# Kernel tuning notes

Measured on AMD Instinct MI355X. Metric: run time of the kernel, lower is better.

The kernel has to match this reference:

```python
import jax, jax.numpy as jnp
import numpy as np

# Segment boundaries from the original hard-coded slices: 13,13,13,9,4 repeated twice
SEG_BOUNDS = [0, 13, 26, 39, 48, 52, 65, 78, 91, 100, 104]


def segmented_log_softmax(x):
    # x: [B, 104]; independent log-softmax over each of the 10 fixed segments
    return jnp.concatenate(
        [jax.nn.log_softmax(x[:, a:b], axis=-1)
         for a, b in zip(SEG_BOUNDS[:-1], SEG_BOUNDS[1:])], axis=-1)


def setup_inputs() -> dict:
    key = jax.random.key(0)
    ks = jax.random.split(key, 8)
    B, H, D = 8192, 2048, 104
    return {
        "line": jax.random.normal(ks[0], (B, D), dtype=jnp.float32),
        "hidden": jax.random.normal(ks[1], (B, H), dtype=jnp.float32),
        "U_w": jax.random.normal(ks[2], (H, H), dtype=jnp.float32) * 0.02,
        "U_b": jax.random.normal(ks[3], (H,), dtype=jnp.float32) * 0.02,
        "W_w": jax.random.normal(ks[4], (H, D), dtype=jnp.float32) * 0.02,
        "W_b": jax.random.normal(ks[5], (H,), dtype=jnp.float32) * 0.02,
        "V_w": jax.random.normal(ks[6], (D, H), dtype=jnp.float32) * 0.02,
        "V_b": jax.random.normal(ks[7], (D,), dtype=jnp.float32) * 0.02,
    }


def reference(line, hidden, U_w, U_b, W_w, W_b, V_w, V_b):
    # h_t = sigmoid(U(hidden) + W(line)); torch Linear: y = x @ W.T + b
    h_t = jax.nn.sigmoid(hidden @ U_w.T + U_b + line @ W_w.T + W_b)  # [B, H]
    pred = h_t @ V_w.T + V_b                                          # [B, 104]
    pred_logsoft = segmented_log_softmax(pred)                        # [B, 104]
    return pred_logsoft, h_t
```

## Files before the change

kernel.cpp:

```cpp
#include <hip/hip_runtime.h>
#include <cstdint>
#include <cstddef>


typedef __bf16 bf16x8 __attribute__((ext_vector_type(8)));
typedef float  f32x4  __attribute__((ext_vector_type(4)));
typedef float  f32x16 __attribute__((ext_vector_type(16)));
typedef int    i32x8  __attribute__((ext_vector_type(8)));
typedef unsigned short ushort8 __attribute__((ext_vector_type(8)));
typedef unsigned char  uchar8  __attribute__((ext_vector_type(8)));
typedef float  float4v __attribute__((ext_vector_type(4)));

#define BB 8192
#define HH 2048
#define DD 104

static __device__ __forceinline__ unsigned short f2bf(float f) {
  unsigned u = __float_as_uint(f);
  unsigned r = (u + 0x7FFFu + ((u >> 16) & 1u)) >> 16;
  return (unsigned short)r;
}

static __device__ __forceinline__ unsigned char f2fp8(float x) {
  unsigned u = __float_as_uint(x);
  unsigned s = (u >> 24) & 0x80u;
  float ax = fabsf(x);
  ax = fminf(ax, 448.0f);
  unsigned code;
  if (ax >= 0.015625f) {
    unsigned b = __float_as_uint(ax);
    unsigned lsb = (b >> 20) & 1u;
    b += 0x0007FFFFu + lsb;
    unsigned e = (b >> 23) & 0xFFu;
    code = ((e - 120u) << 3) | ((b >> 20) & 7u);
  } else {
    code = (unsigned)__float2int_rn(ax * 512.0f);
  }
  return (unsigned char)(s | code);
}

#define GLD_LDS(g, l)                                                          \
  __builtin_amdgcn_global_load_lds(                                            \
      (__attribute__((address_space(1))) void*)(g),                            \
      (__attribute__((address_space(3))) void*)(l), 16, 0, 0)

#define MEMFENCE asm volatile("" ::: "memory")
#define MFMA16(a, b, c) __builtin_amdgcn_mfma_f32_16x16x32_bf16((a), (b), (c), 0, 0, 0)

__global__ __launch_bounds__(256) void conv_fp8_kernel(
    const float* __restrict__ hidden, const float* __restrict__ Uw,
    unsigned char* __restrict__ out_h, unsigned char* __restrict__ out_u) {
  long long i = ((long long)blockIdx.x * blockDim.x + threadIdx.x) * 8;
  const float* src; unsigned char* dst; long long off;
  if (i < (long long)BB * HH) { src = hidden; dst = out_h; off = i; }
  else { src = Uw; dst = out_u; off = i - (long long)BB * HH; }
  float4v a = *(const float4v*)(src + off);
  float4v b = *(const float4v*)(src + off + 4);
  uchar8 o;
  o[0]=f2fp8(a[0]); o[1]=f2fp8(a[1]); o[2]=f2fp8(a[2]); o[3]=f2fp8(a[3]);
  o[4]=f2fp8(b[0]); o[5]=f2fp8(b[1]); o[6]=f2fp8(b[2]); o[7]=f2fp8(b[3]);
  *(uchar8*)(dst + off) = o;
}

__global__ __launch_bounds__(256) void pad_mixed_kernel(
    const float* __restrict__ line, const float* __restrict__ Ww,
    const float* __restrict__ Vw,
    unsigned char* __restrict__ line8, unsigned char* __restrict__ Ww8,
    unsigned short* __restrict__ Vw_bf) {
  int i = blockIdx.x * blockDim.x + threadIdx.x;
  const int N1 = BB * 128;
  const int N2 = N1 + HH * 128;
  if (i < N1) {
    int r = i >> 7, c = i & 127;
    line8[i] = (c < DD) ? f2fp8(line[r * DD + c]) : (unsigned char)0;
  } else if (i < N2) {
    int j = i - N1; int r = j >> 7, c = j & 127;
    Ww8[j] = (c < DD) ? f2fp8(Ww[r * DD + c]) : (unsigned char)0;
  } else {
    int j = i - N2; int r = j >> 11, c = j & 2047;
    Vw_bf[j] = (r < DD) ? f2bf(Vw[r * 2048 + c]) : (unsigned short)0;
  }
}

__global__ __launch_bounds__(256, 2) void gemm1_kernel(
    const unsigned char* __restrict__ A8,
    const unsigned char* __restrict__ L8,
    const unsigned char* __restrict__ U8w,
    const unsigned char* __restrict__ W8w,
    const float* __restrict__ Ub, const float* __restrict__ Wb,
    float* __restrict__ outH, unsigned short* __restrict__ outHbf) {
  __shared__ __attribute__((aligned(32))) unsigned char smem[65536];
  const int t = threadIdx.x;
  const int l = t & 63;
  const int wid = t >> 6;
  const int wr = wid >> 1, wc = wid & 1;

  const int bid = blockIdx.x;
  const int wg = (bid & 7) * 128 + (bid >> 3);
  const int brow = (wg >> 4) * 128;
  const int bcol = (wg & 15) * 128;

  const int lr = l & 31;
  const int lc = l >> 5;

  const int sr = t >> 1, sh = (t & 1) * 16;
  const unsigned char* pA = A8 + (size_t)(brow + sr) * 2048 + sh;
  const unsigned char* pL = L8 + (size_t)(brow + sr) * 128 + sh;
  const unsigned char* pU = U8w + (size_t)(bcol + sr) * 2048 + sh;
  const unsigned char* pW = W8w + (size_t)(bcol + sr) * 128 + sh;
  unsigned char* dA = smem + t * 16;
  unsigned char* dB = smem + 32768 + t * 16;

  f32x16 acc[2][2] = {};

  auto stage = [&](int kt, int buf) {
    const int kb = kt * 128;
    unsigned char* da = dA + buf * 16384;
    unsigned char* db = dB + buf * 16384;
    if (kb < 2048) {
#pragma unroll
      for (int q = 0; q < 4; ++q) {
        GLD_LDS(pA + kb + q * 32, da + q * 4096);
        GLD_LDS(pU + kb + q * 32, db + q * 4096);
      }
    } else {
#pragma unroll
      for (int q = 0; q < 4; ++q) {
        GLD_LDS(pL + q * 32, da + q * 4096);
        GLD_LDS(pW + q * 32, db + q * 4096);
      }
    }
  };

  stage(0, 0);
  asm volatile("s_waitcnt vmcnt(0)" ::: "memory");
  MEMFENCE; __builtin_amdgcn_s_barrier(); MEMFENCE;

  for (int kt = 0; kt < 17; ++kt) {
    const int cur = kt & 1;
    if (kt < 16) {
      stage(kt + 1, cur ^ 1);
      asm volatile("s_waitcnt vmcnt(8)" ::: "memory");
    } else {
      asm volatile("s_waitcnt vmcnt(0)" ::: "memory");
    }
    const unsigned char* Ab = smem + cur * 16384;
    const unsigned char* Bb = smem + 32768 + cur * 16384;
#pragma unroll
    for (int s = 0; s < 2; ++s) {
      const int pr = (s * 2 + lc) * 4096;
      i32x8 af[2], bfv[2];
#pragma unroll
      for (int m = 0; m < 2; ++m)
        af[m] = *(const i32x8*)(Ab + pr + (wr * 64 + m * 32 + lr) * 32);
#pragma unroll
      for (int n = 0; n < 2; ++n)
        bfv[n] = *(const i32x8*)(Bb + pr + (wc * 64 + n * 32 + lr) * 32);
      __builtin_amdgcn_s_setprio(1);
#pragma unroll
      for (int m = 0; m < 2; ++m)
#pragma unroll
        for (int n = 0; n < 2; ++n)
          acc[m][n] = __builtin_amdgcn_mfma_scale_f32_32x32x64_f8f6f4(
              af[m], bfv[n], acc[m][n], 0 , 0 ,
              0, 0x7F7F7F7F , 0, 0x7F7F7F7F );
      __builtin_amdgcn_s_setprio(0);
    }
    MEMFENCE; __builtin_amdgcn_s_barrier(); MEMFENCE;
  }

#pragma unroll
  for (int nf = 0; nf < 2; ++nf) {
    const int col = bcol + wc * 64 + nf * 32 + lr;
    const float bias = Ub[col] + Wb[col];
#pragma unroll
    for (int mf = 0; mf < 2; ++mf) {
#pragma unroll
      for (int reg = 0; reg < 16; ++reg) {
        const int row = brow + wr * 64 + mf * 32 + (reg & 3) + 8 * (reg >> 2) + 4 * lc;
        const float v = acc[mf][nf][reg] + bias;
        const float h = 1.0f / (1.0f + __expf(-v));
        const size_t idx = (size_t)row * HH + col;
        outH[idx] = h;
        outHbf[idx] = f2bf(h);
      }
    }
  }
}

template <int NM, int NN>
static __device__ __forceinline__ void mfma_step(
    const unsigned short* sA, const unsigned short* sB, int arow0, int brow0,
    int frow, int fk, f32x4 (&acc)[NM][NN]) {
  bf16x8 af[NM], bfr[NN];
#pragma unroll
  for (int m = 0; m < NM; ++m)
    af[m] = *(const bf16x8*)(sA + (arow0 + m * 16 + frow) * 32 + fk);
#pragma unroll
  for (int n = 0; n < NN; ++n)
    bfr[n] = *(const bf16x8*)(sB + (brow0 + n * 16 + frow) * 32 + fk);
#pragma unroll
  for (int m = 0; m < NM; ++m)
#pragma unroll
    for (int n = 0; n < NN; ++n)
      acc[m][n] = MFMA16(af[m], bfr[n], acc[m][n]);
}

__global__ __launch_bounds__(256, 2) void gemm2_kernel(
    const unsigned short* __restrict__ A,
    const unsigned short* __restrict__ Bm,
    const float* __restrict__ Vb,
    float* __restrict__ outLS) {
  __shared__ unsigned short sA[64 * 32];
  __shared__ unsigned short sB[128 * 32];
  __shared__ float pred[64 * 105];
  const int t = threadIdx.x;
  const int l = t & 63;
  const int wid = t >> 6, wr = wid >> 1, wc = wid & 1;
  const int brow = blockIdx.x * 64;
  const int srow = t >> 2, scg = t & 3;
  const int frow = l & 15, fk = (l >> 4) * 8;

  const unsigned short* gA = A + (size_t)(brow + srow) * HH + scg * 8;
  const unsigned short* gB = Bm + (size_t)srow * HH + scg * 8;
  unsigned short* lA = sA + t * 8;
  unsigned short* lB = sB + t * 8;

  f32x4 acc[2][4] = {};
  for (int ks = 0; ks < 64; ++ks) {
    __syncthreads();
    GLD_LDS(gA, lA);
    GLD_LDS(gB, lB);
    GLD_LDS(gB + 64 * HH, lB + 64 * 32);
    gA += 32; gB += 32;
    __syncthreads();
    mfma_step<2, 4>(sA, sB, wr * 32, wc * 64, frow, fk, acc);
  }

#pragma unroll
  for (int n = 0; n < 4; ++n) {
    const int col = wc * 64 + n * 16 + frow;
    if (col < DD) {
      const float vb = Vb[col];
#pragma unroll
      for (int m = 0; m < 2; ++m) {
        const int r0 = wr * 32 + m * 16 + (l >> 4) * 4;
#pragma unroll
        for (int j = 0; j < 4; ++j)
          pred[(r0 + j) * 105 + col] = acc[m][n][j] + vb;
      }
    }
  }
  __syncthreads();

  if (t < 64) {
    const int segb[11] = {0, 13, 26, 39, 48, 52, 65, 78, 91, 100, 104};
    const float* p = pred + t * 105;
    float* o = outLS + (size_t)(brow + t) * DD;
    for (int s = 0; s < 10; ++s) {
      const int a = segb[s], b = segb[s + 1];
      float mx = -3.0e38f;
      for (int c = a; c < b; ++c) mx = fmaxf(mx, p[c]);
      float sum = 0.0f;
      for (int c = a; c < b; ++c) sum += __expf(p[c] - mx);
      const float ls = __logf(sum) + mx;
      for (int c = a; c < b; ++c) o[c] = p[c] - ls;
    }
  }
}

extern "C" void kernel_launch(void* const* d_in, const int* in_sizes, int n_in,
                              void* d_out, int out_size, void* d_ws, size_t ws_size,
                              hipStream_t stream) {
  (void)in_sizes; (void)n_in; (void)out_size; (void)ws_size;
  const float* line   = (const float*)d_in[0];
  const float* hidden = (const float*)d_in[1];
  const float* Uw     = (const float*)d_in[2];
  const float* Ub     = (const float*)d_in[3];
  const float* Ww     = (const float*)d_in[4];
  const float* Wb     = (const float*)d_in[5];
  const float* Vw     = (const float*)d_in[6];
  const float* Vb     = (const float*)d_in[7];

  char* ws = (char*)d_ws;
  unsigned char* hid8    = (unsigned char*)(ws);
  unsigned char* U8w     = (unsigned char*)(ws + 16777216);
  unsigned char* line8   = (unsigned char*)(ws + 20971520);
  unsigned char* Ww8     = (unsigned char*)(ws + 22020096);
  unsigned short* Vw_bf  = (unsigned short*)(ws + 22282240);
  unsigned short* ht_bf  = (unsigned short*)(ws + 22806528);

  float* outLS = (float*)d_out;
  float* outH  = (float*)d_out + (size_t)BB * DD;

  conv_fp8_kernel<<<10240, 256, 0, stream>>>(hidden, Uw, hid8, U8w);
  pad_mixed_kernel<<<6144, 256, 0, stream>>>(line, Ww, Vw, line8, Ww8, Vw_bf);
  gemm1_kernel<<<1024, 256, 0, stream>>>(hid8, line8, U8w, Ww8, Ub, Wb,
                                         outH, ht_bf);
  gemm2_kernel<<<128, 256, 0, stream>>>(ht_bf, Vw_bf, Vb, outLS);
}
```

Measured before the change: 117.9 us.

## Halve gemm1 K-tile to 64 and raise occupancy to four blocks per CU

The fp8 GEMM1 kernel now stages 64-wide K tiles instead of 128. That halves LDS use to 32 KB and lets launch bounds request 4 blocks per CU instead of 2. The LDS layout changes so each thread loads one row's 16-byte chunk, and each MFMA fragment is assembled from two 16-byte LDS reads. This doubles the iteration count and the barriers per iteration, adding a barrier before compute, in exchange for more warps to hide latency.

```diff
diff --git a/kernel.cpp b/kernel.cpp
--- a/kernel.cpp
+++ b/kernel.cpp
@@ -6,6 +6,7 @@
 typedef __bf16 bf16x8 __attribute__((ext_vector_type(8)));
 typedef float  f32x4  __attribute__((ext_vector_type(4)));
 typedef float  f32x16 __attribute__((ext_vector_type(16)));
+typedef int    i32x4  __attribute__((ext_vector_type(4)));
 typedef int    i32x8  __attribute__((ext_vector_type(8)));
 typedef unsigned short ushort8 __attribute__((ext_vector_type(8)));
 typedef unsigned char  uchar8  __attribute__((ext_vector_type(8)));
@@ -82,14 +83,24 @@
   }
 }
 
-__global__ __launch_bounds__(256, 2) void gemm1_kernel(
+static __device__ __forceinline__ i32x8 frd(const unsigned char* buf, int row, int lc) {
+  const unsigned char* p = buf + lc * 4096 + row * 16;
+  i32x4 lo = *(const i32x4*)(p);
+  i32x4 hi = *(const i32x4*)(p + 2048);
+  i32x8 r;
+  r[0]=lo[0]; r[1]=lo[1]; r[2]=lo[2]; r[3]=lo[3];
+  r[4]=hi[0]; r[5]=hi[1]; r[6]=hi[2]; r[7]=hi[3];
+  return r;
+}
+
+__global__ __launch_bounds__(256, 4) void gemm1_kernel(
     const unsigned char* __restrict__ A8,
     const unsigned char* __restrict__ L8,
     const unsigned char* __restrict__ U8w,
     const unsigned char* __restrict__ W8w,
     const float* __restrict__ Ub, const float* __restrict__ Wb,
     float* __restrict__ outH, unsigned short* __restrict__ outHbf) {
-  __shared__ __attribute__((aligned(32))) unsigned char smem[65536];
+  __shared__ __attribute__((aligned(16))) unsigned char smem[32768];
   const int t = threadIdx.x;
   const int l = t & 63;
   const int wid = t >> 6;
@@ -103,69 +114,62 @@
   const int lr = l & 31;
   const int lc = l >> 5;
 
-  const int sr = t >> 1, sh = (t & 1) * 16;
-  const unsigned char* pA = A8 + (size_t)(brow + sr) * 2048 + sh;
-  const unsigned char* pL = L8 + (size_t)(brow + sr) * 128 + sh;
-  const unsigned char* pU = U8w + (size_t)(bcol + sr) * 2048 + sh;
-  const unsigned char* pW = W8w + (size_t)(bcol + sr) * 128 + sh;
+  const int sr = t & 127;
+  const int sp = (t >> 7) * 16;
+  const unsigned char* pA = A8 + (size_t)(brow + sr) * 2048 + sp;
+  const unsigned char* pL = L8 + (size_t)(brow + sr) * 128 + sp;
+  const unsigned char* pU = U8w + (size_t)(bcol + sr) * 2048 + sp;
+  const unsigned char* pW = W8w + (size_t)(bcol + sr) * 128 + sp;
   unsigned char* dA = smem + t * 16;
-  unsigned char* dB = smem + 32768 + t * 16;
+  unsigned char* dB = smem + 16384 + t * 16;
 
   f32x16 acc[2][2] = {};
 
   auto stage = [&](int kt, int buf) {
-    const int kb = kt * 128;
-    unsigned char* da = dA + buf * 16384;
-    unsigned char* db = dB + buf * 16384;
+    unsigned char* da = dA + buf * 8192;
+    unsigned char* db = dB + buf * 8192;
+    const int kb = kt * 64;
     if (kb < 2048) {
-#pragma unroll
-      for (int q = 0; q < 4; ++q) {
-        GLD_LDS(pA + kb + q * 32, da + q * 4096);
-        GLD_LDS(pU + kb + q * 32, db + q * 4096);
-      }
+      GLD_LDS(pA + kb, da);
+      GLD_LDS(pA + kb + 32, da + 4096);
+      GLD_LDS(pU + kb, db);
+      GLD_LDS(pU + kb + 32, db + 4096);
     } else {
-#pragma unroll
-      for (int q = 0; q < 4; ++q) {
-        GLD_LDS(pL + q * 32, da + q * 4096);
-        GLD_LDS(pW + q * 32, db + q * 4096);
-      }
+      const int kb2 = kb - 2048;
+      GLD_LDS(pL + kb2, da);
+      GLD_LDS(pL + kb2 + 32, da + 4096);
+      GLD_LDS(pW + kb2, db);
+      GLD_LDS(pW + kb2 + 32, db + 4096);
     }
   };
 
   stage(0, 0);
-  asm volatile("s_waitcnt vmcnt(0)" ::: "memory");
-  MEMFENCE; __builtin_amdgcn_s_barrier(); MEMFENCE;
-
-  for (int kt = 0; kt < 17; ++kt) {
+  for (int kt = 0; kt < 34; ++kt) {
     const int cur = kt & 1;
-    if (kt < 16) {
+    if (kt < 33) {
       stage(kt + 1, cur ^ 1);
-      asm volatile("s_waitcnt vmcnt(8)" ::: "memory");
+      asm volatile("s_waitcnt vmcnt(4)" ::: "memory");
     } else {
       asm volatile("s_waitcnt vmcnt(0)" ::: "memory");
     }
-    const unsigned char* Ab = smem + cur * 16384;
-    const unsigned char* Bb = smem + 32768 + cur * 16384;
-#pragma unroll
-    for (int s = 0; s < 2; ++s) {
-      const int pr = (s * 2 + lc) * 4096;
-      i32x8 af[2], bfv[2];
-#pragma unroll
-      for (int m = 0; m < 2; ++m)
-        af[m] = *(const i32x8*)(Ab + pr + (wr * 64 + m * 32 + lr) * 32);
+    MEMFENCE; __builtin_amdgcn_s_barrier(); MEMFENCE;
+
+    const unsigned char* Ab = smem + cur * 8192;
+    const unsigned char* Bb = smem + 16384 + cur * 8192;
+    i32x8 af[2], bfv[2];
+#pragma unroll
+    for (int m = 0; m < 2; ++m) af[m] = frd(Ab, wr * 64 + m * 32 + lr, lc);
+#pragma unroll
+    for (int n = 0; n < 2; ++n) bfv[n] = frd(Bb, wc * 64 + n * 32 + lr, lc);
+    __builtin_amdgcn_s_setprio(1);
+#pragma unroll
+    for (int m = 0; m < 2; ++m)
 #pragma unroll
       for (int n = 0; n < 2; ++n)
-        bfv[n] = *(const i32x8*)(Bb + pr + (wc * 64 + n * 32 + lr) * 32);
-      __builtin_amdgcn_s_setprio(1);
-#pragma unroll
-      for (int m = 0; m < 2; ++m)
-#pragma unroll
-        for (int n = 0; n < 2; ++n)
-          acc[m][n] = __builtin_amdgcn_mfma_scale_f32_32x32x64_f8f6f4(
-              af[m], bfv[n], acc[m][n], 0 , 0 ,
-              0, 0x7F7F7F7F , 0, 0x7F7F7F7F );
-      __builtin_amdgcn_s_setprio(0);
-    }
+        acc[m][n] = __builtin_amdgcn_mfma_scale_f32_32x32x64_f8f6f4(
+            af[m], bfv[n], acc[m][n], 0 , 0 ,
+            0, 0x7F7F7F7F , 0, 0x7F7F7F7F );
+    __builtin_amdgcn_s_setprio(0);
     MEMFENCE; __builtin_amdgcn_s_barrier(); MEMFENCE;
   }
 
```

After: 154.7 us. 1.31x slower.
